# Optimization experiments

Measured on AMD Instinct MI355X. Metric: run time of the kernel, lower is better.

## Reference

```python
import jax, jax.numpy as jnp
import numpy as np

B, N, E, V, D, H = 16, 4096, 524288, 4, 64, 128
MLP_IN = H + 3 + 2  # node feats + conditioning coords + two temperature scalars
SRC_T, TGT_T = 300.0, 600.0
SCALE_RANGE = 0.5


def _w(k, shape):
    return (jax.random.normal(k, shape, jnp.float32) / np.sqrt(shape[0])).astype(jnp.float32)


def setup_inputs() -> dict:
    key = jax.random.key(0)
    ks = jax.random.split(key, 32)
    inp = {
        "coordinates": jax.random.normal(ks[0], (B, N, 3), jnp.float32),
        "atom_types": jax.random.randint(ks[1], (B, N), 0, V, jnp.int32),
        "adj_list": jax.random.randint(ks[2], (E, 2), 0, N, jnp.int32),
        "edge_batch_idx": jax.random.randint(ks[3], (E,), 0, B, jnp.int32),
        "masked_elements": jnp.zeros((B, N), bool),
        # message-passing GNN params
        "embed": jax.random.normal(ks[4], (V, D), jnp.float32),
        "W_in": _w(ks[5], (D + 3, H)), "b_in": jnp.zeros(H, jnp.float32),
        "W_msg0": _w(ks[6], (2 * H, H)), "b_msg0": jnp.zeros(H, jnp.float32),
        "W_upd0": _w(ks[7], (2 * H, H)), "b_upd0": jnp.zeros(H, jnp.float32),
        "W_msg1": _w(ks[8], (2 * H, H)), "b_msg1": jnp.zeros(H, jnp.float32),
        "W_upd1": _w(ks[9], (2 * H, H)), "b_upd1": jnp.zeros(H, jnp.float32),
        "W_out": _w(ks[10], (H, H)), "b_out": jnp.zeros(H, jnp.float32),
        # scale MLP (random small weights instead of zero init so output is non-trivial)
        "Ws0": _w(ks[11], (MLP_IN, H)), "bs0": jnp.zeros(H, jnp.float32),
        "Ws1": _w(ks[12], (H, H)), "bs1": jnp.zeros(H, jnp.float32),
        "Ws2": _w(ks[13], (H, H // 2)), "bs2": jnp.zeros(H // 2, jnp.float32),
        "Ws3": _w(ks[14], (H // 2, 3)) * 0.1, "bs3": jnp.zeros(3, jnp.float32),
        # shift MLP
        "Wt0": _w(ks[15], (MLP_IN, H)), "bt0": jnp.zeros(H, jnp.float32),
        "Wt1": _w(ks[16], (H, H)), "bt1": jnp.zeros(H, jnp.float32),
        "Wt2": _w(ks[17], (H, H // 2)), "bt2": jnp.zeros(H // 2, jnp.float32),
        "Wt3": _w(ks[18], (H // 2, 3)) * 0.1, "bt3": jnp.zeros(3, jnp.float32),
    }
    return inp


def _mlp(x, layers):
    for Wl, bl in layers[:-1]:
        x = jax.nn.relu(x @ Wl + bl)
    Wl, bl = layers[-1]
    return x @ Wl + bl


def reference(coordinates, atom_types, adj_list, edge_batch_idx, masked_elements,
              embed, W_in, b_in, W_msg0, b_msg0, W_upd0, b_upd0,
              W_msg1, b_msg1, W_upd1, b_upd1, W_out, b_out,
              Ws0, bs0, Ws1, bs1, Ws2, bs2, Ws3, bs3,
              Wt0, bt0, Wt1, bt1, Wt2, bt2, Wt3, bt3):
    Bn, Nn, _ = coordinates.shape
    valid = ~masked_elements                              # [B,N]
    vf = valid[..., None].astype(coordinates.dtype)
    # ---- message passing GNN ----
    h = jnp.concatenate([embed[atom_types], coordinates], -1)  # [B,N,D+3]
    h = jax.nn.relu(h @ W_in + b_in) * vf
    hf = h.reshape(Bn * Nn, -1)
    src = edge_batch_idx * Nn + adj_list[:, 0]
    dst = edge_batch_idx * Nn + adj_list[:, 1]
    for Wm, bm, Wu, bu in ((W_msg0, b_msg0, W_upd0, b_upd0),
                           (W_msg1, b_msg1, W_upd1, b_upd1)):
        m = jax.nn.relu(jnp.concatenate([hf[src], hf[dst]], -1) @ Wm + bm)  # [E,H]
        agg = jax.ops.segment_sum(m, dst, num_segments=Bn * Nn)             # [B*N,H]
        hf = jax.nn.relu(jnp.concatenate([hf, agg], -1) @ Wu + bu)
    node_feats = (hf @ W_out + b_out).reshape(Bn, Nn, -1) * vf              # [B,N,H]
    # ---- coupling transform (phase=0: atoms with type>0 are transformed) ----
    coupling = (atom_types > 0) & valid                  # [B,N]
    cond = coordinates * (~coupling)[..., None].astype(coordinates.dtype)
    temps = jnp.broadcast_to(jnp.asarray([SRC_T, TGT_T], coordinates.dtype), (Bn, Nn, 2))
    x = jnp.concatenate([node_feats, cond, temps], -1)   # [B,N,H+5]
    raw_scales = _mlp(x, [(Ws0, bs0), (Ws1, bs1), (Ws2, bs2), (Ws3, bs3)])
    shifts = _mlp(x, [(Wt0, bt0), (Wt1, bt1), (Wt2, bt2), (Wt3, bt3)])
    m3 = coupling[..., None].astype(coordinates.dtype)   # [B,N,1]
    log_scales = jnp.tanh(raw_scales) * SCALE_RANGE * m3 * vf
    shifts = shifts * m3
    log_det = log_scales.sum((1, 2))                     # [B]
    out = jnp.exp(log_scales) * coordinates + shifts
    out = jnp.where(coupling[..., None], out, coordinates)
    return out, log_det
```

## Files before the change

### kernel.cpp

```cpp
#include <hip/hip_runtime.h>

#define NB    16
#define NN    4096
#define NNODE (NB*NN)
#define NE    524288

typedef __attribute__((ext_vector_type(8))) short bf16x8_t;
typedef __attribute__((ext_vector_type(4))) float f32x4_t;

__device__ __forceinline__ unsigned short f2bf(float f) {
    union { float f; unsigned u; } v; v.f = f;
    return (unsigned short)((v.u + 0x7FFFu + ((v.u >> 16) & 1u)) >> 16);
}
__device__ __forceinline__ float bf2f(unsigned short h) {
    union { unsigned u; float f; } v; v.u = ((unsigned)h) << 16;
    return v.f;
}

__global__ void deg_k(const int* __restrict__ adj, const int* __restrict__ ebi, int* __restrict__ deg)
{
    int e = blockIdx.x * 256 + threadIdx.x;
    atomicAdd(&deg[ebi[e] * NN + adj[2 * e + 1]], 1);
}

// ... 65 lines not shown
        int n = idx >> 7, k = idx & 127;
        WoutP[n * 128 + k] = f2bf(Wout[k * 128 + n]);
    } else if (bid < 768) {
        int idx = (bid - 576) * 256 + tx;
        int n = idx / 192, kk = idx % 192;
        const float* W = n < 128 ? Ws0 : Wt0;
        int nn = n & 127;
        Bt0cat[n * 192 + kk] = f2bf(kk < 133 ? W[kk * 128 + nn] : 0.f);
    } else if (bid < 896) {
        int idx = (bid - 768) * 256 + tx;
        int n = idx >> 7, k = idx & 127;
        const float* W = n < 128 ? Ws1 : Wt1;
        Bt1cat[n * 128 + k] = f2bf(W[k * 128 + (n & 127)]);
    } else if (bid < 1024) {
        int idx = (bid - 896) * 256 + tx;
        int n = idx >> 7, k = idx & 127;
        const float* W = n < 128 ? Ws2 : Wt2;
        int nn = n & 127;
        Bt2cat[n * 128 + k] = f2bf(nn < 64 ? W[k * 64 + nn] : 0.f);
    } else if (bid == 1024) {
        b0cat[tx] = (tx < 128) ? bs0[tx] : bt0[tx - 128];
    } else if (bid == 1025) {
        b1cat[tx] = (tx < 128) ? bs1[tx] : bt1[tx - 128];
    } else if (bid == 1026) {
        int nn = tx & 127;
        b2cat[tx] = (nn < 64) ? ((tx < 128) ? bs2[nn] : bt2[nn]) : 0.f;
    } else if (bid == 1027) {
        bm0cat[tx] = (tx < 128) ? 0.f : bm0[tx - 128];
    } else {
        bm1cat[tx] = (tx < 128) ? 0.f : bm1[tx - 128];
    }
}

__device__ __forceinline__ void msg_phase(const char* act, char* Bs,
    const unsigned short* __restrict__ Bt, const float* __restrict__ bias,
    unsigned short* __restrict__ P12, size_t row0, int tx)
{
    const int wid = tx >> 6, l = tx & 63;
    const int wr = wid >> 1, wc = wid & 1;
    const int rsel = l & 15, kq = l >> 4;
    const int rg = l >> 4, cc = l & 15;
#pragma unroll
    for (int nh = 0; nh < 2; ++nh) {
        f32x4_t acc[2][4];
#pragma unroll
        for (int i = 0; i < 2; ++i)
#pragma unroll
            for (int j = 0; j < 4; ++j) { f32x4_t z = {0.f,0.f,0.f,0.f}; acc[i][j] = z; }
#pragma unroll
        for (int kc = 0; kc < 128; kc += 64) {
            __syncthreads();
#pragma unroll
            for (int p = 0; p < 4; ++p) {
                int idx = tx + p * 256;
                int n = idx >> 3, kg = idx & 7;
                uint4 v = *(const uint4*)(Bt + (size_t)(nh * 128 + n) * 128 + kc + kg * 8);
                *(uint4*)(Bs + n * 128 + ((kg * 16) ^ ((n & 7) << 4))) = v;
            }
            __syncthreads();
#pragma unroll
            for (int ks = 0; ks < 2; ++ks) {
                bf16x8_t af[2], bv[4];
#pragma unroll
                for (int fm = 0; fm < 2; ++fm) {
                    int r = wr * 32 + fm * 16 + rsel;
                    af[fm] = *(const bf16x8_t*)(act + r * 256 + kc * 2 + ((ks * 64 + kq * 16) ^ ((r & 7) << 4)));
                }
#pragma unroll
                for (int fn = 0; fn < 4; ++fn) {
                    int n = wc * 64 + fn * 16 + rsel;
                    bv[fn] = *(const bf16x8_t*)(Bs + n * 128 + ((ks * 64 + kq * 16) ^ ((n & 7) << 4)));
                }
#pragma unroll
                for (int fm = 0; fm < 2; ++fm)
#pragma unroll
                    for (int fn = 0; fn < 4; ++fn)
                        acc[fm][fn] = __builtin_amdgcn_mfma_f32_16x16x32_bf16(af[fm], bv[fn], acc[fm][fn], 0, 0, 0);
            }
        }
        __syncthreads();
#pragma unroll
        for (int fm = 0; fm < 2; ++fm)
#pragma unroll
            for (int rr = 0; rr < 4; ++rr) {
                int row = wr * 32 + fm * 16 + rg * 4 + rr;
#pragma unroll
                for (int fn = 0; fn < 4; ++fn) {
                    int col = wc * 64 + fn * 16 + cc;
                    float v = acc[fm][fn][rr] + bias[nh * 128 + col];
                    int cb = col * 2;
                    *(unsigned short*)(Bs + row * 256 + (cb & ~127) + ((cb & 127) ^ ((row & 7) << 4))) = f2bf(v);
                }
            }
        __syncthreads();
#pragma unroll
        for (int p = 0; p < 4; ++p) {
            int idx = tx + p * 256;
            int row = idx >> 4, g = idx & 15;
            int pb = g * 16;
            uint4 v = *(const uint4*)(Bs + row * 256 + (pb & ~127) + ((pb & 127) ^ ((row & 7) << 4)));
            *(uint4*)(P12 + (row0 + row) * 256 + nh * 128 + g * 8) = v;
        }
    }
}

__launch_bounds__(256, 4)
__global__ void fused_im_k(const int* __restrict__ types, const float* __restrict__ coords,
                           const unsigned char* __restrict__ maskb,
                           const float* __restrict__ embed, const float* __restrict__ W_in,
                           const float* __restrict__ b_in,
                           const unsigned short* __restrict__ Btm, const float* __restrict__ bmcat,
                           unsigned short* __restrict__ hf, unsigned short* __restrict__ P12)
{
    __shared__ __align__(16) char act[16384];
    __shared__ __align__(16) char Bs[16384];
    const int tx = threadIdx.x;
    const size_t row0 = (size_t)blockIdx.x * 64;

    float* wf = (float*)Bs;
    float* xs = (float*)(Bs + 4096);
#pragma unroll
    for (int p = 0; p < 4; ++p) {
        int idx = tx + p * 256;
        int k = idx >> 7, c = idx & 127;
        wf[idx] = (k < 7) ? W_in[k * 128 + c] : b_in[c];
    }
    if (tx < 64) {
        size_t node = row0 + tx;
        int tp = types[node];
#pragma unroll
        for (int j = 0; j < 4; ++j) xs[tx * 8 + j] = embed[(size_t)tp * 4 + j];
#pragma unroll
        for (int j = 0; j < 3; ++j) xs[tx * 8 + 4 + j] = coords[node * 3 + j];
    }
    __syncthreads();
    {
        int row = tx >> 2, c0 = (tx & 3) * 32;
        float x0 = xs[row*8+0], x1 = xs[row*8+1], x2 = xs[row*8+2], x3 = xs[row*8+3];
        float x4 = xs[row*8+4], x5 = xs[row*8+5], x6 = xs[row*8+6];
        bool msk = maskb[row0 + row];
        int swz = (row & 7) << 4;
#pragma unroll
        for (int c = 0; c < 32; ++c) {
            int col = c0 + c;
            float a = wf[7*128+col] + x0*wf[col] + x1*wf[128+col] + x2*wf[256+col]
                    + x3*wf[384+col] + x4*wf[512+col] + x5*wf[640+col] + x6*wf[768+col];
            a = msk ? 0.f : fmaxf(a, 0.f);
            int cb = col * 2;
            *(unsigned short*)(act + row * 256 + (cb & ~127) + ((cb & 127) ^ swz)) = f2bf(a);
        }
    }
    __syncthreads();
#pragma unroll
    for (int p = 0; p < 4; ++p) {
        int idx = tx + p * 256;
        int row = idx >> 4, g = idx & 15;
        int pb = g * 16;
        uint4 v = *(const uint4*)(act + row * 256 + (pb & ~127) + ((pb & 127) ^ ((row & 7) << 4)));
        *(uint4*)(hf + (row0 + row) * 128 + g * 8) = v;
    }
    msg_phase(act, Bs, Btm, bmcat, P12, row0, tx);
}

__launch_bounds__(256, 4)
__global__ void fused_um_k(const unsigned short* __restrict__ hfin,
                           const unsigned short* __restrict__ aggp,
                           const unsigned short* __restrict__ Btu, const float* __restrict__ bu,
                           const unsigned short* __restrict__ Btm, const float* __restrict__ bmcat,
                           unsigned short* __restrict__ hfout, unsigned short* __restrict__ P12)
{
    __shared__ __align__(16) char act[16384];
    __shared__ __align__(16) char Bs[16384];
    const int tx = threadIdx.x;
    const int wid = tx >> 6, l = tx & 63;
    const int wr = wid >> 1, wc = wid & 1;
    const int rsel = l & 15, kq = l >> 4, rg = l >> 4, cc = l & 15;
    const size_t row0 = (size_t)blockIdx.x * 64;

    f32x4_t acc[2][4];
#pragma unroll
    for (int i = 0; i < 2; ++i)
#pragma unroll
        for (int j = 0; j < 4; ++j) { f32x4_t z = {0.f,0.f,0.f,0.f}; acc[i][j] = z; }
#pragma unroll
    for (int kc = 0; kc < 256; kc += 64) {
        const unsigned short* Ap = (kc < 128) ? hfin : aggp;
        int kloc = (kc < 128) ? kc : kc - 128;
        __syncthreads();
#pragma unroll
        for (int p = 0; p < 4; ++p) {
            int idx = tx + p * 256;
            int n = idx >> 3, kg = idx & 7;
            uint4 v = *(const uint4*)(Btu + (size_t)n * 256 + kc + kg * 8);
            *(uint4*)(Bs + n * 128 + ((kg * 16) ^ ((n & 7) << 4))) = v;
        }
        __syncthreads();
#pragma unroll
        for (int ks = 0; ks < 2; ++ks) {
            bf16x8_t af[2], bv[4];
#pragma unroll
            for (int fm = 0; fm < 2; ++fm) {
                size_t r = row0 + wr * 32 + fm * 16 + rsel;
                af[fm] = *(const bf16x8_t*)(Ap + r * 128 + kloc + ks * 32 + kq * 8);
            }
#pragma unroll
            for (int fn = 0; fn < 4; ++fn) {
                int n = wc * 64 + fn * 16 + rsel;
                bv[fn] = *(const bf16x8_t*)(Bs + n * 128 + ((ks * 64 + kq * 16) ^ ((n & 7) << 4)));
            }
#pragma unroll
            for (int fm = 0; fm < 2; ++fm)
#pragma unroll
                for (int fn = 0; fn < 4; ++fn)
                    acc[fm][fn] = __builtin_amdgcn_mfma_f32_16x16x32_bf16(af[fm], bv[fn], acc[fm][fn], 0, 0, 0);
        }
    }
#pragma unroll
    for (int fm = 0; fm < 2; ++fm)
#pragma unroll
        for (int rr = 0; rr < 4; ++rr) {
            int row = wr * 32 + fm * 16 + rg * 4 + rr;
#pragma unroll
            for (int fn = 0; fn < 4; ++fn) {
                int col = wc * 64 + fn * 16 + cc;
                float v = fmaxf(acc[fm][fn][rr] + bu[col], 0.f);
                int cb = col * 2;
                *(unsigned short*)(act + row * 256 + (cb & ~127) + ((cb & 127) ^ ((row & 7) << 4))) = f2bf(v);
            }
        }
    __syncthreads();
#pragma unroll
    for (int p = 0; p < 4; ++p) {
        int idx = tx + p * 256;
        int row = idx >> 4, g = idx & 15;
        int pb = g * 16;
        uint4 v = *(const uint4*)(act + row * 256 + (pb & ~127) + ((pb & 127) ^ ((row & 7) << 4)));
        *(uint4*)(hfout + (row0 + row) * 128 + g * 8) = v;
    }
    msg_phase(act, Bs, Btm, bmcat, P12, row0, tx);
}

__global__ void agg_k(const unsigned short* __restrict__ P12,
                      const int* __restrict__ offs, const int* __restrict__ esrc,
                      unsigned short* __restrict__ agg)
{
    int bid = blockIdx.x;
    int chunk = gridDim.x >> 3;
    int swz = (bid & 7) * chunk + (bid >> 3);
    int node = swz * 4 + (threadIdx.x >> 6);
    int l = threadIdx.x & 63;
    int beg = offs[node], end = offs[node + 1];
    unsigned p2w = *(const unsigned*)(P12 + (size_t)node * 256 + 128 + 2 * l);
    float p2a = bf2f((unsigned short)(p2w & 0xFFFF));
    float p2b = bf2f((unsigned short)(p2w >> 16));
    float aa = 0.f, ab = 0.f;
    int i = beg;
    for (; i + 3 < end; i += 4) {
        int s0 = esrc[i], s1 = esrc[i+1], s2 = esrc[i+2], s3 = esrc[i+3];
        unsigned v0 = *(const unsigned*)(P12 + (size_t)s0 * 256 + 2 * l);
        unsigned v1 = *(const unsigned*)(P12 + (size_t)s1 * 256 + 2 * l);
        unsigned v2 = *(const unsigned*)(P12 + (size_t)s2 * 256 + 2 * l);
        unsigned v3 = *(const unsigned*)(P12 + (size_t)s3 * 256 + 2 * l);
        aa += fmaxf(bf2f((unsigned short)(v0 & 0xFFFF)) + p2a, 0.f);
        ab += fmaxf(bf2f((unsigned short)(v0 >> 16))    + p2b, 0.f);
        aa += fmaxf(bf2f((unsigned short)(v1 & 0xFFFF)) + p2a, 0.f);
        ab += fmaxf(bf2f((unsigned short)(v1 >> 16))    + p2b, 0.f);
        aa += fmaxf(bf2f((unsigned short)(v2 & 0xFFFF)) + p2a, 0.f);
        ab += fmaxf(bf2f((unsigned short)(v2 >> 16))    + p2b, 0.f);
        aa += fmaxf(bf2f((unsigned short)(v3 & 0xFFFF)) + p2a, 0.f);
        ab += fmaxf(bf2f((unsigned short)(v3 >> 16))    + p2b, 0.f);
    }
    for (; i < end; ++i) {
        int s0 = esrc[i];
        unsigned v0 = *(const unsigned*)(P12 + (size_t)s0 * 256 + 2 * l);
        aa += fmaxf(bf2f((unsigned short)(v0 & 0xFFFF)) + p2a, 0.f);
        ab += fmaxf(bf2f((unsigned short)(v0 >> 16))    + p2b, 0.f);
    }
    unsigned o = (unsigned)f2bf(aa) | ((unsigned)f2bf(ab) << 16);
    *(unsigned*)(agg + (size_t)node * 128 + 2 * l) = o;
}

__launch_bounds__(256, 2)
__global__ void fused_ut_k(const unsigned short* __restrict__ hfin,
                           const unsigned short* __restrict__ aggp,
                           const unsigned short* __restrict__ Btu, const float* __restrict__ bu,
                           const unsigned short* __restrict__ WoutP, const float* __restrict__ bOut,
                           const unsigned short* __restrict__ Bt0, const float* __restrict__ b0,
                           const unsigned short* __restrict__ Bt1, const float* __restrict__ b1,
                           const unsigned short* __restrict__ Bt2, const float* __restrict__ b2,
                           const float* __restrict__ Ws3, const float* __restrict__ bs3,
                           const float* __restrict__ Wt3, const float* __restrict__ bt3,
                           const float* __restrict__ coords, const int* __restrict__ types,
                           const unsigned char* __restrict__ maskb,
                           float* __restrict__ outc, float* __restrict__ partial)
{
    __shared__ __align__(16) char act[32768];
    __shared__ __align__(16) char hfn[16384];
    __shared__ __align__(16) char Bs[32768];
    const int tx = threadIdx.x;
    const int wid = tx >> 6, l = tx & 63;
    const int rsel = l & 15, kq = l >> 4, rg = l >> 4, cc = l & 15;
    const size_t row0 = (size_t)blockIdx.x * 64;

    {
        const int wr = wid >> 1, wc = wid & 1;
        f32x4_t acc[2][4];
#pragma unroll
        for (int i = 0; i < 2; ++i)
#pragma unroll
            for (int j = 0; j < 4; ++j) { f32x4_t z = {0.f,0.f,0.f,0.f}; acc[i][j] = z; }
#pragma unroll
        for (int kc = 0; kc < 256; kc += 64) {
            const unsigned short* Ap = (kc < 128) ? hfin : aggp;
            int kloc = (kc < 128) ? kc : kc - 128;
            __syncthreads();
#pragma unroll
            for (int p = 0; p < 4; ++p) {
                int idx = tx + p * 256;
                int n = idx >> 3, kg = idx & 7;
                uint4 v = *(const uint4*)(Btu + (size_t)n * 256 + kc + kg * 8);
                *(uint4*)(Bs + n * 128 + ((kg * 16) ^ ((n & 7) << 4))) = v;
            }
            __syncthreads();
#pragma unroll
            for (int ks = 0; ks < 2; ++ks) {
                bf16x8_t af[2], bv[4];
#pragma unroll
                for (int fm = 0; fm < 2; ++fm) {
                    size_t r = row0 + wr * 32 + fm * 16 + rsel;
                    af[fm] = *(const bf16x8_t*)(Ap + r * 128 + kloc + ks * 32 + kq * 8);
                }
#pragma unroll
                for (int fn = 0; fn < 4; ++fn) {
                    int n = wc * 64 + fn * 16 + rsel;
                    bv[fn] = *(const bf16x8_t*)(Bs + n * 128 + ((ks * 64 + kq * 16) ^ ((n & 7) << 4)));
                }
#pragma unroll
                for (int fm = 0; fm < 2; ++fm)
#pragma unroll
                    for (int fn = 0; fn < 4; ++fn)
                        acc[fm][fn] = __builtin_amdgcn_mfma_f32_16x16x32_bf16(af[fm], bv[fn], acc[fm][fn], 0, 0, 0);
            }
        }
#pragma unroll
        for (int fm = 0; fm < 2; ++fm)
#pragma unroll
            for (int rr = 0; rr < 4; ++rr) {
                int row = wr * 32 + fm * 16 + rg * 4 + rr;
#pragma unroll
                for (int fn = 0; fn < 4; ++fn) {
                    int col = wc * 64 + fn * 16 + cc;
                    float v = fmaxf(acc[fm][fn][rr] + bu[col], 0.f);
                    int cb = col * 2;
                    *(unsigned short*)(hfn + row * 256 + (cb & ~127) + ((cb & 127) ^ ((row & 7) << 4))) = f2bf(v);
                }
            }
    }
    __syncthreads();

    {
        const int wr = wid >> 1, wc = wid & 1;
        f32x4_t acc[2][4];
#pragma unroll
        for (int i = 0; i < 2; ++i)
#pragma unroll
            for (int j = 0; j < 4; ++j) { f32x4_t z = {0.f,0.f,0.f,0.f}; acc[i][j] = z; }
#pragma unroll
        for (int kc = 0; kc < 128; kc += 64) {
            __syncthreads();
#pragma unroll
            for (int p = 0; p < 4; ++p) {
                int idx = tx + p * 256;
                int n = idx >> 3, kg = idx & 7;
                uint4 v = *(const uint4*)(WoutP + (size_t)n * 128 + kc + kg * 8);
                *(uint4*)(Bs + n * 128 + ((kg * 16) ^ ((n & 7) << 4))) = v;
            }
            __syncthreads();
#pragma unroll
            for (int ks = 0; ks < 2; ++ks) {
                bf16x8_t af[2], bv[4];
#pragma unroll
                for (int fm = 0; fm < 2; ++fm) {
                    int r = wr * 32 + fm * 16 + rsel;
                    af[fm] = *(const bf16x8_t*)(hfn + r * 256 + kc * 2 + ((ks * 64 + kq * 16) ^ ((r & 7) << 4)));
                }
#pragma unroll
                for (int fn = 0; fn < 4; ++fn) {
                    int n = wc * 64 + fn * 16 + rsel;
                    bv[fn] = *(const bf16x8_t*)(Bs + n * 128 + ((ks * 64 + kq * 16) ^ ((n & 7) << 4)));
                }
#pragma unroll
                for (int fm = 0; fm < 2; ++fm)
#pragma unroll
                    for (int fn = 0; fn < 4; ++fn)
                        acc[fm][fn] = __builtin_amdgcn_mfma_f32_16x16x32_bf16(af[fm], bv[fn], acc[fm][fn], 0, 0, 0);
            }
        }
#pragma unroll
        for (int fm = 0; fm < 2; ++fm)
#pragma unroll
            for (int rr = 0; rr < 4; ++rr) {
                int row = wr * 32 + fm * 16 + rg * 4 + rr;
                bool zero = maskb[row0 + row];
#pragma unroll
                for (int fn = 0; fn < 4; ++fn) {
                    int col = wc * 64 + fn * 16 + cc;
                    float v = acc[fm][fn][rr] + bOut[col];
                    if (zero) v = 0.f;
                    int cb = col * 2;
                    *(unsigned short*)(act + row * 512 + (cb & ~127) + ((cb & 127) ^ ((row & 7) << 4))) = f2bf(v);
                }
            }
    }
#pragma unroll
    for (int p = 0; p < 16; ++p) {
        int idx = tx + p * 256;
        int row = idx >> 6, ci = idx & 63;
        int col = 128 + ci;
        size_t node = row0 + row;
        bool coup = (types[node] > 0) && !maskb[node];
        float v;
        if (ci < 3)       v = coup ? 0.f : coords[node * 3 + ci];
        else if (ci == 3) v = 300.f;
        else if (ci == 4) v = 600.f;
        else              v = 0.f;
        int cb = col * 2;
        *(unsigned short*)(act + row * 512 + (cb & ~127) + ((cb & 127) ^ ((row & 7) << 4))) = f2bf(v);
    }
    __syncthreads();

    const int wr = wid >> 1, wc = wid & 1;
#pragma unroll
    for (int layer = 0; layer < 3; ++layer) {
        const unsigned short* Bt = layer == 0 ? Bt0 : (layer == 1 ? Bt1 : Bt2);
        const float* bb = layer == 0 ? b0 : (layer == 1 ? b1 : b2);
        const int ldbt = layer == 0 ? 192 : 128;
        const int Ktot = layer == 0 ? 192 : 128;
        const int kbase = (layer == 0) ? 0 : (wc ? 256 : 0);
        f32x4_t acc[2][8];
#pragma unroll
        for (int i = 0; i < 2; ++i)
#pragma unroll
            for (int j = 0; j < 8; ++j) { f32x4_t z = {0.f,0.f,0.f,0.f}; acc[i][j] = z; }
        for (int kc = 0; kc < Ktot; kc += 64) {
            __syncthreads();
#pragma unroll
            for (int p = 0; p < 8; ++p) {
                int idx = tx + p * 256;
                int n = idx >> 3, kg = idx & 7;
                uint4 v = *(const uint4*)(Bt + (size_t)n * ldbt + kc + kg * 8);
                *(uint4*)(Bs + n * 128 + ((kg * 16) ^ ((n & 7) << 4))) = v;
            }
            __syncthreads();
#pragma unroll
            for (int ks = 0; ks < 2; ++ks) {
                bf16x8_t af[2], bv[8];
#pragma unroll
                for (int fm = 0; fm < 2; ++fm) {
                    int r = wr * 32 + fm * 16 + rsel;
                    af[fm] = *(const bf16x8_t*)(act + r * 512 + kbase + kc * 2 + ((ks * 64 + kq * 16) ^ ((r & 7) << 4)));
                }
#pragma unroll
                for (int fn = 0; fn < 8; ++fn) {
                    int n = wc * 128 + fn * 16 + rsel;
                    bv[fn] = *(const bf16x8_t*)(Bs + n * 128 + ((ks * 64 + kq * 16) ^ ((n & 7) << 4)));
                }
#pragma unroll
                for (int fm = 0; fm < 2; ++fm)
#pragma unroll
                    for (int fn = 0; fn < 8; ++fn)
                        acc[fm][fn] = __builtin_amdgcn_mfma_f32_16x16x32_bf16(af[fm], bv[fn], acc[fm][fn], 0, 0, 0);
            }
        }
        __syncthreads();
#pragma unroll
        for (int fm = 0; fm < 2; ++fm)
#pragma unroll
            for (int rr = 0; rr < 4; ++rr) {
                int row = wr * 32 + fm * 16 + rg * 4 + rr;
#pragma unroll
                for (int fn = 0; fn < 8; ++fn) {
                    int col = wc * 128 + fn * 16 + cc;
                    float v = fmaxf(acc[fm][fn][rr] + bb[col], 0.f);
                    int cb = col * 2;
                    *(unsigned short*)(act + row * 512 + (cb & ~127) + ((cb & 127) ^ ((row & 7) << 4))) = f2bf(v);
                }
            }
        __syncthreads();
    }

    float* W3f = (float*)hfn;
    float* red = (float*)(hfn + 2048);
    for (int i = tx; i < 384; i += 256)
        W3f[i] = (i < 192) ? Ws3[i] : Wt3[i - 192];
    __syncthreads();
    {
        int row = tx >> 2, sub = tx & 3;
        int swz = (row & 7) << 4;
        float rs0 = 0.f, rs1 = 0.f, rs2 = 0.f, sh0 = 0.f, sh1 = 0.f, sh2 = 0.f;
#pragma unroll
        for (int kk = 0; kk < 16; ++kk) {
            int k = sub * 16 + kk;
            float av = bf2f(*(const unsigned short*)(act + row * 512 + ((k * 2) ^ swz)));
            float bv = bf2f(*(const unsigned short*)(act + row * 512 + 256 + ((k * 2) ^ swz)));
            rs0 += av * W3f[k * 3 + 0]; rs1 += av * W3f[k * 3 + 1]; rs2 += av * W3f[k * 3 + 2];
            sh0 += bv * W3f[192 + k * 3 + 0]; sh1 += bv * W3f[192 + k * 3 + 1]; sh2 += bv * W3f[192 + k * 3 + 2];
        }
        rs0 += __shfl_xor(rs0, 1); rs0 += __shfl_xor(rs0, 2);
        rs1 += __shfl_xor(rs1, 1); rs1 += __shfl_xor(rs1, 2);
        rs2 += __shfl_xor(rs2, 1); rs2 += __shfl_xor(rs2, 2);
        sh0 += __shfl_xor(sh0, 1); sh0 += __shfl_xor(sh0, 2);
        sh1 += __shfl_xor(sh1, 1); sh1 += __shfl_xor(sh1, 2);
        sh2 += __shfl_xor(sh2, 1); sh2 += __shfl_xor(sh2, 2);
        if (sub == 0) {
            size_t node = row0 + row;
            bool coup = (types[node] > 0) && !maskb[node];
            float c0 = coords[node * 3 + 0], c1 = coords[node * 3 + 1], c2 = coords[node * 3 + 2];
            float ls0 = 0.f, ls1 = 0.f, ls2 = 0.f, o0 = c0, o1 = c1, o2 = c2;
            if (coup) {
                ls0 = tanhf(rs0 + bs3[0]) * 0.5f;
// ... 68 lines not shown
    int*   offs = (int*)alloc((size_t)(NNODE + 1) * 4);
    int*   cur  = (int*)alloc((size_t)NNODE * 4);
    int*   esrc = (int*)alloc((size_t)NE * 4);
    unsigned short* Btm0 = (unsigned short*)alloc(256 * 128 * 2);
    unsigned short* Btm1 = (unsigned short*)alloc(256 * 128 * 2);
    unsigned short* Btu0 = (unsigned short*)alloc(128 * 256 * 2);
    unsigned short* Btu1 = (unsigned short*)alloc(128 * 256 * 2);
    unsigned short* WoutP  = (unsigned short*)alloc(128 * 128 * 2);
    unsigned short* Bt0cat = (unsigned short*)alloc(256 * 192 * 2);
    unsigned short* Bt1cat = (unsigned short*)alloc(256 * 128 * 2);
    unsigned short* Bt2cat = (unsigned short*)alloc(256 * 128 * 2);
    float* b0cat  = (float*)alloc(256 * 4);
    float* b1cat  = (float*)alloc(256 * 4);
    float* b2cat  = (float*)alloc(256 * 4);
    float* bm0cat = (float*)alloc(256 * 4);
    float* bm1cat = (float*)alloc(256 * 4);
    float* partial = (float*)alloc(1024 * 4);

    hipMemsetAsync(deg, 0, (size_t)NNODE * 4, stream);
    hipMemsetAsync(cur, 0, (size_t)NNODE * 4, stream);

    deg_k<<<NE / 256, 256, 0, stream>>>(adj, ebi, deg);
    scan_k<<<1, 1024, 0, stream>>>(deg, offs);
    scat_k<<<NE / 256, 256, 0, stream>>>(adj, ebi, offs, cur, esrc);
    prep_k<<<1029, 256, 0, stream>>>(W_msg[0], W_msg[1], W_upd[0], W_upd[1], W_out,
                                     Ws0, Wt0, Ws1, Wt1, Ws2, Wt2,
                                     bs0, bt0, bs1, bt1, bs2, bt2, b_msg[0], b_msg[1],
                                     Btm0, Btm1, Btu0, Btu1, WoutP,
                                     Bt0cat, Bt1cat, Bt2cat,
                                     b0cat, b1cat, b2cat, bm0cat, bm1cat);

    fused_im_k<<<1024, 256, 0, stream>>>(types, coords, maskb, embed, W_in, b_in,
                                         Btm0, bm0cat, hf, P12);
    agg_k<<<NNODE / 4, 256, 0, stream>>>(P12, offs, esrc, agg);
    fused_um_k<<<1024, 256, 0, stream>>>(hf, agg, Btu0, b_upd[0], Btm1, bm1cat, hf, P12);
    agg_k<<<NNODE / 4, 256, 0, stream>>>(P12, offs, esrc, agg);

    float* outc = (float*)d_out;
    fused_ut_k<<<1024, 256, 0, stream>>>(hf, agg, Btu1, b_upd[1], WoutP, b_out,
                                         Bt0cat, b0cat, Bt1cat, b1cat, Bt2cat, b2cat,
                                         Ws3, bs3, Wt3, bt3,
                                         coords, types, maskb, outc, partial);
    red_k<<<1, 256, 0, stream>>>(partial, outc + (size_t)NNODE * 3);
}
```

Baseline: 260.1 us.

## Load GEMM weight fragments directly from global memory instead of staging through LDS

Every MFMA GEMM loop in the message, update and tail kernels now reads its B-operand fragments straight from global memory (served by L1/L2 for the small, shared weight matrices) instead of copying weight tiles into a shared Bs buffer with two barriers per K-chunk. This removes the per-chunk LDS staging stores and __syncthreads, and drops the 32 KB Bs buffer from the tail kernel. The tail kernel's launch bound is raised from 2 to 3 blocks per CU to use the freed LDS. The cost is more global/cache load traffic per wave, with longer load latency sitting directly in front of the MFMAs and no software prefetch to hide it.

```diff
diff --git a/kernel.cpp b/kernel.cpp
--- a/kernel.cpp
+++ b/kernel.cpp
@@ -121,7 +121,7 @@
     }
 }
 
-__device__ __forceinline__ void msg_phase(const char* act, char* Bs,
+__device__ __forceinline__ void msg_phase(const char* act, char* buf,
     const unsigned short* __restrict__ Bt, const float* __restrict__ bias,
     unsigned short* __restrict__ P12, size_t row0, int tx)
 {
@@ -137,35 +137,24 @@
 #pragma unroll
             for (int j = 0; j < 4; ++j) { f32x4_t z = {0.f,0.f,0.f,0.f}; acc[i][j] = z; }
 #pragma unroll
-        for (int kc = 0; kc < 128; kc += 64) {
-            __syncthreads();
-#pragma unroll
-            for (int p = 0; p < 4; ++p) {
-                int idx = tx + p * 256;
-                int n = idx >> 3, kg = idx & 7;
-                uint4 v = *(const uint4*)(Bt + (size_t)(nh * 128 + n) * 128 + kc + kg * 8);
-                *(uint4*)(Bs + n * 128 + ((kg * 16) ^ ((n & 7) << 4))) = v;
-            }
-            __syncthreads();
-#pragma unroll
-            for (int ks = 0; ks < 2; ++ks) {
-                bf16x8_t af[2], bv[4];
-#pragma unroll
-                for (int fm = 0; fm < 2; ++fm) {
-                    int r = wr * 32 + fm * 16 + rsel;
-                    af[fm] = *(const bf16x8_t*)(act + r * 256 + kc * 2 + ((ks * 64 + kq * 16) ^ ((r & 7) << 4)));
-                }
-#pragma unroll
-                for (int fn = 0; fn < 4; ++fn) {
-                    int n = wc * 64 + fn * 16 + rsel;
-                    bv[fn] = *(const bf16x8_t*)(Bs + n * 128 + ((ks * 64 + kq * 16) ^ ((n & 7) << 4)));
-                }
-#pragma unroll
-                for (int fm = 0; fm < 2; ++fm)
-#pragma unroll
-                    for (int fn = 0; fn < 4; ++fn)
-                        acc[fm][fn] = __builtin_amdgcn_mfma_f32_16x16x32_bf16(af[fm], bv[fn], acc[fm][fn], 0, 0, 0);
-            }
+        for (int kk = 0; kk < 128; kk += 32) {
+            bf16x8_t af[2], bv[4];
+#pragma unroll
+            for (int fm = 0; fm < 2; ++fm) {
+                int r = wr * 32 + fm * 16 + rsel;
+                int ab = (kk + kq * 8) * 2;
+                af[fm] = *(const bf16x8_t*)(act + r * 256 + (ab & ~127) + ((ab & 127) ^ ((r & 7) << 4)));
+            }
+#pragma unroll
+            for (int fn = 0; fn < 4; ++fn) {
+                int n = nh * 128 + wc * 64 + fn * 16 + rsel;
+                bv[fn] = *(const bf16x8_t*)(Bt + (size_t)n * 128 + kk + kq * 8);
+            }
+#pragma unroll
+            for (int fm = 0; fm < 2; ++fm)
+#pragma unroll
+                for (int fn = 0; fn < 4; ++fn)
+                    acc[fm][fn] = __builtin_amdgcn_mfma_f32_16x16x32_bf16(af[fm], bv[fn], acc[fm][fn], 0, 0, 0);
         }
         __syncthreads();
 #pragma unroll
@@ -178,7 +167,7 @@
                     int col = wc * 64 + fn * 16 + cc;
                     float v = acc[fm][fn][rr] + bias[nh * 128 + col];
                     int cb = col * 2;
-                    *(unsigned short*)(Bs + row * 256 + (cb & ~127) + ((cb & 127) ^ ((row & 7) << 4))) = f2bf(v);
+                    *(unsigned short*)(buf + row * 256 + (cb & ~127) + ((cb & 127) ^ ((row & 7) << 4))) = f2bf(v);
                 }
             }
         __syncthreads();
@@ -187,7 +176,7 @@
             int idx = tx + p * 256;
             int row = idx >> 4, g = idx & 15;
             int pb = g * 16;
-            uint4 v = *(const uint4*)(Bs + row * 256 + (pb & ~127) + ((pb & 127) ^ ((row & 7) << 4)));
+            uint4 v = *(const uint4*)(buf + row * 256 + (pb & ~127) + ((pb & 127) ^ ((row & 7) << 4)));
             *(uint4*)(P12 + (row0 + row) * 256 + nh * 128 + g * 8) = v;
         }
     }
@@ -202,12 +191,12 @@
                            unsigned short* __restrict__ hf, unsigned short* __restrict__ P12)
 {
     __shared__ __align__(16) char act[16384];
-    __shared__ __align__(16) char Bs[16384];
+    __shared__ __align__(16) char buf[16384];
     const int tx = threadIdx.x;
     const size_t row0 = (size_t)blockIdx.x * 64;
 
-    float* wf = (float*)Bs;
-    float* xs = (float*)(Bs + 4096);
+    float* wf = (float*)buf;
+    float* xs = (float*)(buf + 4096);
 #pragma unroll
     for (int p = 0; p < 4; ++p) {
         int idx = tx + p * 256;
@@ -248,7 +237,7 @@
         uint4 v = *(const uint4*)(act + row * 256 + (pb & ~127) + ((pb & 127) ^ ((row & 7) << 4)));
         *(uint4*)(hf + (row0 + row) * 128 + g * 8) = v;
     }
-    msg_phase(act, Bs, Btm, bmcat, P12, row0, tx);
+    msg_phase(act, buf, Btm, bmcat, P12, row0, tx);
 }
 
 __launch_bounds__(256, 4)
@@ -259,7 +248,7 @@
                            unsigned short* __restrict__ hfout, unsigned short* __restrict__ P12)
 {
     __shared__ __align__(16) char act[16384];
-    __shared__ __align__(16) char Bs[16384];
+    __shared__ __align__(16) char buf[16384];
     const int tx = threadIdx.x;
     const int wid = tx >> 6, l = tx & 63;
     const int wr = wid >> 1, wc = wid & 1;
@@ -272,37 +261,25 @@
 #pragma unroll
         for (int j = 0; j < 4; ++j) { f32x4_t z = {0.f,0.f,0.f,0.f}; acc[i][j] = z; }
 #pragma unroll
-    for (int kc = 0; kc < 256; kc += 64) {
-        const unsigned short* Ap = (kc < 128) ? hfin : aggp;
-        int kloc = (kc < 128) ? kc : kc - 128;
-        __syncthreads();
-#pragma unroll
-        for (int p = 0; p < 4; ++p) {
-            int idx = tx + p * 256;
-            int n = idx >> 3, kg = idx & 7;
-            uint4 v = *(const uint4*)(Btu + (size_t)n * 256 + kc + kg * 8);
-            *(uint4*)(Bs + n * 128 + ((kg * 16) ^ ((n & 7) << 4))) = v;
-        }
-        __syncthreads();
-#pragma unroll
-        for (int ks = 0; ks < 2; ++ks) {
-            bf16x8_t af[2], bv[4];
-#pragma unroll
-            for (int fm = 0; fm < 2; ++fm) {
-                size_t r = row0 + wr * 32 + fm * 16 + rsel;
-                af[fm] = *(const bf16x8_t*)(Ap + r * 128 + kloc + ks * 32 + kq * 8);
-            }
-#pragma unroll
-            for (int fn = 0; fn < 4; ++fn) {
-                int n = wc * 64 + fn * 16 + rsel;
-                bv[fn] = *(const bf16x8_t*)(Bs + n * 128 + ((ks * 64 + kq * 16) ^ ((n & 7) << 4)));
-            }
-#pragma unroll
-            for (int fm = 0; fm < 2; ++fm)
-#pragma unroll
-                for (int fn = 0; fn < 4; ++fn)
-                    acc[fm][fn] = __builtin_amdgcn_mfma_f32_16x16x32_bf16(af[fm], bv[fn], acc[fm][fn], 0, 0, 0);
-        }
+    for (int kk = 0; kk < 256; kk += 32) {
+        const unsigned short* Ap = (kk < 128) ? hfin : aggp;
+        int kloc = kk & 127;
+        bf16x8_t af[2], bv[4];
+#pragma unroll
+        for (int fm = 0; fm < 2; ++fm) {
+            size_t r = row0 + wr * 32 + fm * 16 + rsel;
+            af[fm] = *(const bf16x8_t*)(Ap + r * 128 + kloc + kq * 8);
+        }
+#pragma unroll
+        for (int fn = 0; fn < 4; ++fn) {
+            int n = wc * 64 + fn * 16 + rsel;
+            bv[fn] = *(const bf16x8_t*)(Btu + (size_t)n * 256 + kk + kq * 8);
+        }
+#pragma unroll
+        for (int fm = 0; fm < 2; ++fm)
+#pragma unroll
+            for (int fn = 0; fn < 4; ++fn)
+                acc[fm][fn] = __builtin_amdgcn_mfma_f32_16x16x32_bf16(af[fm], bv[fn], acc[fm][fn], 0, 0, 0);
     }
 #pragma unroll
     for (int fm = 0; fm < 2; ++fm)
@@ -326,7 +303,7 @@
         uint4 v = *(const uint4*)(act + row * 256 + (pb & ~127) + ((pb & 127) ^ ((row & 7) << 4)));
         *(uint4*)(hfout + (row0 + row) * 128 + g * 8) = v;
     }
-    msg_phase(act, Bs, Btm, bmcat, P12, row0, tx);
+    msg_phase(act, buf, Btm, bmcat, P12, row0, tx);
 }
 
 __global__ void agg_k(const unsigned short* __restrict__ P12,
@@ -369,7 +346,7 @@
     *(unsigned*)(agg + (size_t)node * 128 + 2 * l) = o;
 }
 
-__launch_bounds__(256, 2)
+__launch_bounds__(256, 3)
 __global__ void fused_ut_k(const unsigned short* __restrict__ hfin,
                            const unsigned short* __restrict__ aggp,
                            const unsigned short* __restrict__ Btu, const float* __restrict__ bu,
@@ -385,51 +362,38 @@
 {
     __shared__ __align__(16) char act[32768];
     __shared__ __align__(16) char hfn[16384];
-    __shared__ __align__(16) char Bs[32768];
     const int tx = threadIdx.x;
     const int wid = tx >> 6, l = tx & 63;
     const int rsel = l & 15, kq = l >> 4, rg = l >> 4, cc = l & 15;
     const size_t row0 = (size_t)blockIdx.x * 64;
+    const int wr = wid >> 1, wc = wid & 1;
 
     {
-        const int wr = wid >> 1, wc = wid & 1;
         f32x4_t acc[2][4];
 #pragma unroll
         for (int i = 0; i < 2; ++i)
 #pragma unroll
             for (int j = 0; j < 4; ++j) { f32x4_t z = {0.f,0.f,0.f,0.f}; acc[i][j] = z; }
 #pragma unroll
-        for (int kc = 0; kc < 256; kc += 64) {
-            const unsigned short* Ap = (kc < 128) ? hfin : aggp;
-            int kloc = (kc < 128) ? kc : kc - 128;
-            __syncthreads();
-#pragma unroll
-            for (int p = 0; p < 4; ++p) {
-                int idx = tx + p * 256;
-                int n = idx >> 3, kg = idx & 7;
-                uint4 v = *(const uint4*)(Btu + (size_t)n * 256 + kc + kg * 8);
-                *(uint4*)(Bs + n * 128 + ((kg * 16) ^ ((n & 7) << 4))) = v;
-            }
-            __syncthreads();
-#pragma unroll
-            for (int ks = 0; ks < 2; ++ks) {
-                bf16x8_t af[2], bv[4];
-#pragma unroll
-                for (int fm = 0; fm < 2; ++fm) {
-                    size_t r = row0 + wr * 32 + fm * 16 + rsel;
-                    af[fm] = *(const bf16x8_t*)(Ap + r * 128 + kloc + ks * 32 + kq * 8);
-                }
-#pragma unroll
-                for (int fn = 0; fn < 4; ++fn) {
-                    int n = wc * 64 + fn * 16 + rsel;
-                    bv[fn] = *(const bf16x8_t*)(Bs + n * 128 + ((ks * 64 + kq * 16) ^ ((n & 7) << 4)));
-                }
-#pragma unroll
-                for (int fm = 0; fm < 2; ++fm)
-#pragma unroll
-                    for (int fn = 0; fn < 4; ++fn)
-                        acc[fm][fn] = __builtin_amdgcn_mfma_f32_16x16x32_bf16(af[fm], bv[fn], acc[fm][fn], 0, 0, 0);
-            }
+        for (int kk = 0; kk < 256; kk += 32) {
+            const unsigned short* Ap = (kk < 128) ? hfin : aggp;
+            int kloc = kk & 127;
+            bf16x8_t af[2], bv[4];
+#pragma unroll
+            for (int fm = 0; fm < 2; ++fm) {
+                size_t r = row0 + wr * 32 + fm * 16 + rsel;
+                af[fm] = *(const bf16x8_t*)(Ap + r * 128 + kloc + kq * 8);
+            }
+#pragma unroll
+            for (int fn = 0; fn < 4; ++fn) {
+                int n = wc * 64 + fn * 16 + rsel;
+                bv[fn] = *(const bf16x8_t*)(Btu + (size_t)n * 256 + kk + kq * 8);
+            }
+#pragma unroll
+            for (int fm = 0; fm < 2; ++fm)
+#pragma unroll
+                for (int fn = 0; fn < 4; ++fn)
+                    acc[fm][fn] = __builtin_amdgcn_mfma_f32_16x16x32_bf16(af[fm], bv[fn], acc[fm][fn], 0, 0, 0);
         }
 #pragma unroll
         for (int fm = 0; fm < 2; ++fm)
@@ -448,42 +412,30 @@
     __syncthreads();
 
     {
-        const int wr = wid >> 1, wc = wid & 1;
         f32x4_t acc[2][4];
 #pragma unroll
         for (int i = 0; i < 2; ++i)
 #pragma unroll
             for (int j = 0; j < 4; ++j) { f32x4_t z = {0.f,0.f,0.f,0.f}; acc[i][j] = z; }
 #pragma unroll
-        for (int kc = 0; kc < 128; kc += 64) {
-            __syncthreads();
-#pragma unroll
-            for (int p = 0; p < 4; ++p) {
-                int idx = tx + p * 256;
-                int n = idx >> 3, kg = idx & 7;
-                uint4 v = *(const uint4*)(WoutP + (size_t)n * 128 + kc + kg * 8);
-                *(uint4*)(Bs + n * 128 + ((kg * 16) ^ ((n & 7) << 4))) = v;
-            }
-            __syncthreads();
-#pragma unroll
-            for (int ks = 0; ks < 2; ++ks) {
-                bf16x8_t af[2], bv[4];
-#pragma unroll
-                for (int fm = 0; fm < 2; ++fm) {
-                    int r = wr * 32 + fm * 16 + rsel;
-                    af[fm] = *(const bf16x8_t*)(hfn + r * 256 + kc * 2 + ((ks * 64 + kq * 16) ^ ((r & 7) << 4)));
-                }
-#pragma unroll
-                for (int fn = 0; fn < 4; ++fn) {
-                    int n = wc * 64 + fn * 16 + rsel;
-                    bv[fn] = *(const bf16x8_t*)(Bs + n * 128 + ((ks * 64 + kq * 16) ^ ((n & 7) << 4)));
-                }
-#pragma unroll
-                for (int fm = 0; fm < 2; ++fm)
-#pragma unroll
-                    for (int fn = 0; fn < 4; ++fn)
-                        acc[fm][fn] = __builtin_amdgcn_mfma_f32_16x16x32_bf16(af[fm], bv[fn], acc[fm][fn], 0, 0, 0);
-            }
+        for (int kk = 0; kk < 128; kk += 32) {
+            bf16x8_t af[2], bv[4];
+#pragma unroll
+            for (int fm = 0; fm < 2; ++fm) {
+                int r = wr * 32 + fm * 16 + rsel;
+                int ab = (kk + kq * 8) * 2;
+                af[fm] = *(const bf16x8_t*)(hfn + r * 256 + (ab & ~127) + ((ab & 127) ^ ((r & 7) << 4)));
+            }
+#pragma unroll
+            for (int fn = 0; fn < 4; ++fn) {
+                int n = wc * 64 + fn * 16 + rsel;
+                bv[fn] = *(const bf16x8_t*)(WoutP + (size_t)n * 128 + kk + kq * 8);
+            }
+#pragma unroll
+            for (int fm = 0; fm < 2; ++fm)
+#pragma unroll
+                for (int fn = 0; fn < 4; ++fn)
+                    acc[fm][fn] = __builtin_amdgcn_mfma_f32_16x16x32_bf16(af[fm], bv[fn], acc[fm][fn], 0, 0, 0);
         }
 #pragma unroll
         for (int fm = 0; fm < 2; ++fm)
@@ -518,7 +470,6 @@
     }
     __syncthreads();
 
-    const int wr = wid >> 1, wc = wid & 1;
 #pragma unroll
     for (int layer = 0; layer < 3; ++layer) {
         const unsigned short* Bt = layer == 0 ? Bt0 : (layer == 1 ? Bt1 : Bt2);
@@ -531,35 +482,24 @@
         for (int i = 0; i < 2; ++i)
 #pragma unroll
             for (int j = 0; j < 8; ++j) { f32x4_t z = {0.f,0.f,0.f,0.f}; acc[i][j] = z; }
-        for (int kc = 0; kc < Ktot; kc += 64) {
-            __syncthreads();
-#pragma unroll
-            for (int p = 0; p < 8; ++p) {
-                int idx = tx + p * 256;
-                int n = idx >> 3, kg = idx & 7;
-                uint4 v = *(const uint4*)(Bt + (size_t)n * ldbt + kc + kg * 8);
-                *(uint4*)(Bs + n * 128 + ((kg * 16) ^ ((n & 7) << 4))) = v;
-            }
-            __syncthreads();
-#pragma unroll
-            for (int ks = 0; ks < 2; ++ks) {
-                bf16x8_t af[2], bv[8];
-#pragma unroll
-                for (int fm = 0; fm < 2; ++fm) {
-                    int r = wr * 32 + fm * 16 + rsel;
-                    af[fm] = *(const bf16x8_t*)(act + r * 512 + kbase + kc * 2 + ((ks * 64 + kq * 16) ^ ((r & 7) << 4)));
-                }
-#pragma unroll
-                for (int fn = 0; fn < 8; ++fn) {
-                    int n = wc * 128 + fn * 16 + rsel;
-                    bv[fn] = *(const bf16x8_t*)(Bs + n * 128 + ((ks * 64 + kq * 16) ^ ((n & 7) << 4)));
-                }
-#pragma unroll
-                for (int fm = 0; fm < 2; ++fm)
-#pragma unroll
-                    for (int fn = 0; fn < 8; ++fn)
-                        acc[fm][fn] = __builtin_amdgcn_mfma_f32_16x16x32_bf16(af[fm], bv[fn], acc[fm][fn], 0, 0, 0);
-            }
+        for (int kk = 0; kk < Ktot; kk += 32) {
+            bf16x8_t af[2], bv[8];
+#pragma unroll
+            for (int fm = 0; fm < 2; ++fm) {
+                int r = wr * 32 + fm * 16 + rsel;
+                int ab = (kk + kq * 8) * 2;
+                af[fm] = *(const bf16x8_t*)(act + r * 512 + kbase + (ab & ~127) + ((ab & 127) ^ ((r & 7) << 4)));
+            }
+#pragma unroll
+            for (int fn = 0; fn < 8; ++fn) {
+                int n = wc * 128 + fn * 16 + rsel;
+                bv[fn] = *(const bf16x8_t*)(Bt + (size_t)n * ldbt + kk + kq * 8);
+            }
+#pragma unroll
+            for (int fm = 0; fm < 2; ++fm)
+#pragma unroll
+                for (int fn = 0; fn < 8; ++fn)
+                    acc[fm][fn] = __builtin_amdgcn_mfma_f32_16x16x32_bf16(af[fm], bv[fn], acc[fm][fn], 0, 0, 0);
         }
         __syncthreads();
 #pragma unroll
```

Result: slower. 367.8 us (+41.4%).

## Halve agg threads per node with wider loads; cut fused_ut LDS for occupancy

Applied to the files above, without the earlier changes.

The aggregation kernel now gives each node 32 lanes that each load 8 bytes (four bf16 features) per neighbour, so one block covers 8 nodes and launches half as many blocks. The final fused update/MLP kernel drops its separate 32 KB B-tile buffer: it reuses the activation buffer for the first GEMMs and splits the MLP layer GEMMs into two 128-column halves staged through the 16 KB hfn buffer. Launch bounds are raised to 3 blocks per SM to raise occupancy. This adds extra barriers and half-width tile reloads, and staging B into act before act holds the activations depends on the exact order of barriers.

```diff
diff --git a/kernel.cpp b/kernel.cpp
--- a/kernel.cpp
+++ b/kernel.cpp
@@ -274,7 +274,7 @@
 #pragma unroll
     for (int kc = 0; kc < 256; kc += 64) {
         const unsigned short* Ap = (kc < 128) ? hfin : aggp;
-        int kloc = (kc < 128) ? kc : kc - 128;
+        int kloc = kc & 127;
         __syncthreads();
 #pragma unroll
         for (int p = 0; p < 4; ++p) {
@@ -336,40 +336,54 @@
     int bid = blockIdx.x;
     int chunk = gridDim.x >> 3;
     int swz = (bid & 7) * chunk + (bid >> 3);
-    int node = swz * 4 + (threadIdx.x >> 6);
-    int l = threadIdx.x & 63;
+    int node = swz * 8 + (threadIdx.x >> 5);
+    int l = threadIdx.x & 31;
     int beg = offs[node], end = offs[node + 1];
-    unsigned p2w = *(const unsigned*)(P12 + (size_t)node * 256 + 128 + 2 * l);
-    float p2a = bf2f((unsigned short)(p2w & 0xFFFF));
-    float p2b = bf2f((unsigned short)(p2w >> 16));
-    float aa = 0.f, ab = 0.f;
+    uint2 p2w = *(const uint2*)(P12 + (size_t)node * 256 + 128 + 4 * l);
+    float p2a = bf2f((unsigned short)(p2w.x & 0xFFFF));
+    float p2b = bf2f((unsigned short)(p2w.x >> 16));
+    float p2c = bf2f((unsigned short)(p2w.y & 0xFFFF));
+    float p2d = bf2f((unsigned short)(p2w.y >> 16));
+    float aa = 0.f, ab = 0.f, ac = 0.f, ad = 0.f;
     int i = beg;
     for (; i + 3 < end; i += 4) {
         int s0 = esrc[i], s1 = esrc[i+1], s2 = esrc[i+2], s3 = esrc[i+3];
-        unsigned v0 = *(const unsigned*)(P12 + (size_t)s0 * 256 + 2 * l);
-        unsigned v1 = *(const unsigned*)(P12 + (size_t)s1 * 256 + 2 * l);
-        unsigned v2 = *(const unsigned*)(P12 + (size_t)s2 * 256 + 2 * l);
-        unsigned v3 = *(const unsigned*)(P12 + (size_t)s3 * 256 + 2 * l);
-        aa += fmaxf(bf2f((unsigned short)(v0 & 0xFFFF)) + p2a, 0.f);
-        ab += fmaxf(bf2f((unsigned short)(v0 >> 16))    + p2b, 0.f);
-        aa += fmaxf(bf2f((unsigned short)(v1 & 0xFFFF)) + p2a, 0.f);
-        ab += fmaxf(bf2f((unsigned short)(v1 >> 16))    + p2b, 0.f);
-        aa += fmaxf(bf2f((unsigned short)(v2 & 0xFFFF)) + p2a, 0.f);
-        ab += fmaxf(bf2f((unsigned short)(v2 >> 16))    + p2b, 0.f);
-        aa += fmaxf(bf2f((unsigned short)(v3 & 0xFFFF)) + p2a, 0.f);
-        ab += fmaxf(bf2f((unsigned short)(v3 >> 16))    + p2b, 0.f);
+        uint2 v0 = *(const uint2*)(P12 + (size_t)s0 * 256 + 4 * l);
+        uint2 v1 = *(const uint2*)(P12 + (size_t)s1 * 256 + 4 * l);
+        uint2 v2 = *(const uint2*)(P12 + (size_t)s2 * 256 + 4 * l);
+        uint2 v3 = *(const uint2*)(P12 + (size_t)s3 * 256 + 4 * l);
+        aa += fmaxf(bf2f((unsigned short)(v0.x & 0xFFFF)) + p2a, 0.f);
+        ab += fmaxf(bf2f((unsigned short)(v0.x >> 16))    + p2b, 0.f);
+        ac += fmaxf(bf2f((unsigned short)(v0.y & 0xFFFF)) + p2c, 0.f);
+        ad += fmaxf(bf2f((unsigned short)(v0.y >> 16))    + p2d, 0.f);
+        aa += fmaxf(bf2f((unsigned short)(v1.x & 0xFFFF)) + p2a, 0.f);
+        ab += fmaxf(bf2f((unsigned short)(v1.x >> 16))    + p2b, 0.f);
+        ac += fmaxf(bf2f((unsigned short)(v1.y & 0xFFFF)) + p2c, 0.f);
+        ad += fmaxf(bf2f((unsigned short)(v1.y >> 16))    + p2d, 0.f);
+        aa += fmaxf(bf2f((unsigned short)(v2.x & 0xFFFF)) + p2a, 0.f);
+        ab += fmaxf(bf2f((unsigned short)(v2.x >> 16))    + p2b, 0.f);
+        ac += fmaxf(bf2f((unsigned short)(v2.y & 0xFFFF)) + p2c, 0.f);
+        ad += fmaxf(bf2f((unsigned short)(v2.y >> 16))    + p2d, 0.f);
+        aa += fmaxf(bf2f((unsigned short)(v3.x & 0xFFFF)) + p2a, 0.f);
+        ab += fmaxf(bf2f((unsigned short)(v3.x >> 16))    + p2b, 0.f);
+        ac += fmaxf(bf2f((unsigned short)(v3.y & 0xFFFF)) + p2c, 0.f);
+        ad += fmaxf(bf2f((unsigned short)(v3.y >> 16))    + p2d, 0.f);
     }
     for (; i < end; ++i) {
         int s0 = esrc[i];
-        unsigned v0 = *(const unsigned*)(P12 + (size_t)s0 * 256 + 2 * l);
-        aa += fmaxf(bf2f((unsigned short)(v0 & 0xFFFF)) + p2a, 0.f);
-        ab += fmaxf(bf2f((unsigned short)(v0 >> 16))    + p2b, 0.f);
-    }
-    unsigned o = (unsigned)f2bf(aa) | ((unsigned)f2bf(ab) << 16);
-    *(unsigned*)(agg + (size_t)node * 128 + 2 * l) = o;
-}
-
-__launch_bounds__(256, 2)
+        uint2 v0 = *(const uint2*)(P12 + (size_t)s0 * 256 + 4 * l);
+        aa += fmaxf(bf2f((unsigned short)(v0.x & 0xFFFF)) + p2a, 0.f);
+        ab += fmaxf(bf2f((unsigned short)(v0.x >> 16))    + p2b, 0.f);
+        ac += fmaxf(bf2f((unsigned short)(v0.y & 0xFFFF)) + p2c, 0.f);
+        ad += fmaxf(bf2f((unsigned short)(v0.y >> 16))    + p2d, 0.f);
+    }
+    uint2 o;
+    o.x = (unsigned)f2bf(aa) | ((unsigned)f2bf(ab) << 16);
+    o.y = (unsigned)f2bf(ac) | ((unsigned)f2bf(ad) << 16);
+    *(uint2*)(agg + (size_t)node * 128 + 4 * l) = o;
+}
+
+__launch_bounds__(256, 3)
 __global__ void fused_ut_k(const unsigned short* __restrict__ hfin,
                            const unsigned short* __restrict__ aggp,
                            const unsigned short* __restrict__ Btu, const float* __restrict__ bu,
@@ -385,14 +399,13 @@
 {
     __shared__ __align__(16) char act[32768];
     __shared__ __align__(16) char hfn[16384];
-    __shared__ __align__(16) char Bs[32768];
     const int tx = threadIdx.x;
     const int wid = tx >> 6, l = tx & 63;
     const int rsel = l & 15, kq = l >> 4, rg = l >> 4, cc = l & 15;
     const size_t row0 = (size_t)blockIdx.x * 64;
+    const int wr = wid >> 1, wc = wid & 1;
 
     {
-        const int wr = wid >> 1, wc = wid & 1;
         f32x4_t acc[2][4];
 #pragma unroll
         for (int i = 0; i < 2; ++i)
@@ -401,14 +414,14 @@
 #pragma unroll
         for (int kc = 0; kc < 256; kc += 64) {
             const unsigned short* Ap = (kc < 128) ? hfin : aggp;
-            int kloc = (kc < 128) ? kc : kc - 128;
+            int kloc = kc & 127;
             __syncthreads();
 #pragma unroll
             for (int p = 0; p < 4; ++p) {
                 int idx = tx + p * 256;
                 int n = idx >> 3, kg = idx & 7;
                 uint4 v = *(const uint4*)(Btu + (size_t)n * 256 + kc + kg * 8);
-                *(uint4*)(Bs + n * 128 + ((kg * 16) ^ ((n & 7) << 4))) = v;
+                *(uint4*)(act + n * 128 + ((kg * 16) ^ ((n & 7) << 4))) = v;
             }
             __syncthreads();
 #pragma unroll
@@ -422,7 +435,7 @@
 #pragma unroll
                 for (int fn = 0; fn < 4; ++fn) {
                     int n = wc * 64 + fn * 16 + rsel;
-                    bv[fn] = *(const bf16x8_t*)(Bs + n * 128 + ((ks * 64 + kq * 16) ^ ((n & 7) << 4)));
+                    bv[fn] = *(const bf16x8_t*)(act + n * 128 + ((ks * 64 + kq * 16) ^ ((n & 7) << 4)));
                 }
 #pragma unroll
                 for (int fm = 0; fm < 2; ++fm)
@@ -445,10 +458,8 @@
                 }
             }
     }
-    __syncthreads();
 
     {
-        const int wr = wid >> 1, wc = wid & 1;
         f32x4_t acc[2][4];
 #pragma unroll
         for (int i = 0; i < 2; ++i)
@@ -462,7 +473,7 @@
                 int idx = tx + p * 256;
                 int n = idx >> 3, kg = idx & 7;
                 uint4 v = *(const uint4*)(WoutP + (size_t)n * 128 + kc + kg * 8);
-                *(uint4*)(Bs + n * 128 + ((kg * 16) ^ ((n & 7) << 4))) = v;
+                *(uint4*)(act + n * 128 + ((kg * 16) ^ ((n & 7) << 4))) = v;
             }
             __syncthreads();
 #pragma unroll
@@ -476,7 +487,7 @@
 #pragma unroll
                 for (int fn = 0; fn < 4; ++fn) {
                     int n = wc * 64 + fn * 16 + rsel;
-                    bv[fn] = *(const bf16x8_t*)(Bs + n * 128 + ((ks * 64 + kq * 16) ^ ((n & 7) << 4)));
+                    bv[fn] = *(const bf16x8_t*)(act + n * 128 + ((ks * 64 + kq * 16) ^ ((n & 7) << 4)));
                 }
 #pragma unroll
                 for (int fm = 0; fm < 2; ++fm)
@@ -485,6 +496,7 @@
                         acc[fm][fn] = __builtin_amdgcn_mfma_f32_16x16x32_bf16(af[fm], bv[fn], acc[fm][fn], 0, 0, 0);
             }
         }
+        __syncthreads();
 #pragma unroll
         for (int fm = 0; fm < 2; ++fm)
 #pragma unroll
@@ -518,63 +530,69 @@
     }
     __syncthreads();
 
-    const int wr = wid >> 1, wc = wid & 1;
 #pragma unroll
     for (int layer = 0; layer < 3; ++layer) {
         const unsigned short* Bt = layer == 0 ? Bt0 : (layer == 1 ? Bt1 : Bt2);
         const float* bb = layer == 0 ? b0 : (layer == 1 ? b1 : b2);
         const int ldbt = layer == 0 ? 192 : 128;
         const int Ktot = layer == 0 ? 192 : 128;
-        const int kbase = (layer == 0) ? 0 : (wc ? 256 : 0);
-        f32x4_t acc[2][8];
-#pragma unroll
-        for (int i = 0; i < 2; ++i)
-#pragma unroll
-            for (int j = 0; j < 8; ++j) { f32x4_t z = {0.f,0.f,0.f,0.f}; acc[i][j] = z; }
+        f32x4_t acc[2][2][4];
+#pragma unroll
+        for (int h = 0; h < 2; ++h)
+#pragma unroll
+            for (int i = 0; i < 2; ++i)
+#pragma unroll
+                for (int j = 0; j < 4; ++j) { f32x4_t z = {0.f,0.f,0.f,0.f}; acc[h][i][j] = z; }
         for (int kc = 0; kc < Ktot; kc += 64) {
-            __syncthreads();
-#pragma unroll
-            for (int p = 0; p < 8; ++p) {
-                int idx = tx + p * 256;
-                int n = idx >> 3, kg = idx & 7;
-                uint4 v = *(const uint4*)(Bt + (size_t)n * ldbt + kc + kg * 8);
-                *(uint4*)(Bs + n * 128 + ((kg * 16) ^ ((n & 7) << 4))) = v;
-            }
-            __syncthreads();
-#pragma unroll
-            for (int ks = 0; ks < 2; ++ks) {
-                bf16x8_t af[2], bv[8];
-#pragma unroll
-                for (int fm = 0; fm < 2; ++fm) {
-                    int r = wr * 32 + fm * 16 + rsel;
-                    af[fm] = *(const bf16x8_t*)(act + r * 512 + kbase + kc * 2 + ((ks * 64 + kq * 16) ^ ((r & 7) << 4)));
-                }
-#pragma unroll
-                for (int fn = 0; fn < 8; ++fn) {
-                    int n = wc * 128 + fn * 16 + rsel;
-                    bv[fn] = *(const bf16x8_t*)(Bs + n * 128 + ((ks * 64 + kq * 16) ^ ((n & 7) << 4)));
-                }
-#pragma unroll
-                for (int fm = 0; fm < 2; ++fm)
-#pragma unroll
-                    for (int fn = 0; fn < 8; ++fn)
-                        acc[fm][fn] = __builtin_amdgcn_mfma_f32_16x16x32_bf16(af[fm], bv[fn], acc[fm][fn], 0, 0, 0);
-            }
-        }
-        __syncthreads();
-#pragma unroll
-        for (int fm = 0; fm < 2; ++fm)
-#pragma unroll
-            for (int rr = 0; rr < 4; ++rr) {
-                int row = wr * 32 + fm * 16 + rg * 4 + rr;
-#pragma unroll
-                for (int fn = 0; fn < 8; ++fn) {
-                    int col = wc * 128 + fn * 16 + cc;
-                    float v = fmaxf(acc[fm][fn][rr] + bb[col], 0.f);
-                    int cb = col * 2;
-                    *(unsigned short*)(act + row * 512 + (cb & ~127) + ((cb & 127) ^ ((row & 7) << 4))) = f2bf(v);
-                }
-            }
+#pragma unroll
+            for (int h = 0; h < 2; ++h) {
+                __syncthreads();
+#pragma unroll
+                for (int p = 0; p < 4; ++p) {
+                    int idx = tx + p * 256;
+                    int n = idx >> 3, kg = idx & 7;
+                    uint4 v = *(const uint4*)(Bt + (size_t)(h * 128 + n) * ldbt + kc + kg * 8);
+                    *(uint4*)(hfn + n * 128 + ((kg * 16) ^ ((n & 7) << 4))) = v;
+                }
+                __syncthreads();
+                const int kbase = (layer == 0) ? 0 : (h ? 256 : 0);
+#pragma unroll
+                for (int ks = 0; ks < 2; ++ks) {
+                    bf16x8_t af[2], bv[4];
+#pragma unroll
+                    for (int fm = 0; fm < 2; ++fm) {
+                        int r = wr * 32 + fm * 16 + rsel;
+                        af[fm] = *(const bf16x8_t*)(act + r * 512 + kbase + kc * 2 + ((ks * 64 + kq * 16) ^ ((r & 7) << 4)));
+                    }
+#pragma unroll
+                    for (int fn = 0; fn < 4; ++fn) {
+                        int n = wc * 64 + fn * 16 + rsel;
+                        bv[fn] = *(const bf16x8_t*)(hfn + n * 128 + ((ks * 64 + kq * 16) ^ ((n & 7) << 4)));
+                    }
+#pragma unroll
+                    for (int fm = 0; fm < 2; ++fm)
+#pragma unroll
+                        for (int fn = 0; fn < 4; ++fn)
+                            acc[h][fm][fn] = __builtin_amdgcn_mfma_f32_16x16x32_bf16(af[fm], bv[fn], acc[h][fm][fn], 0, 0, 0);
+                }
+            }
+        }
+        __syncthreads();
+#pragma unroll
+        for (int h = 0; h < 2; ++h)
+#pragma unroll
+            for (int fm = 0; fm < 2; ++fm)
+#pragma unroll
+                for (int rr = 0; rr < 4; ++rr) {
+                    int row = wr * 32 + fm * 16 + rg * 4 + rr;
+#pragma unroll
+                    for (int fn = 0; fn < 4; ++fn) {
+                        int col = h * 128 + wc * 64 + fn * 16 + cc;
+                        float v = fmaxf(acc[h][fm][fn][rr] + bb[col], 0.f);
+                        int cb = col * 2;
+                        *(unsigned short*)(act + row * 512 + (cb & ~127) + ((cb & 127) ^ ((row & 7) << 4))) = f2bf(v);
+                    }
+                }
         __syncthreads();
     }
 
@@ -709,9 +727,9 @@
 
     fused_im_k<<<1024, 256, 0, stream>>>(types, coords, maskb, embed, W_in, b_in,
                                          Btm0, bm0cat, hf, P12);
-    agg_k<<<NNODE / 4, 256, 0, stream>>>(P12, offs, esrc, agg);
+    agg_k<<<NNODE / 8, 256, 0, stream>>>(P12, offs, esrc, agg);
     fused_um_k<<<1024, 256, 0, stream>>>(hf, agg, Btu0, b_upd[0], Btm1, bm1cat, hf, P12);
-    agg_k<<<NNODE / 4, 256, 0, stream>>>(P12, offs, esrc, agg);
+    agg_k<<<NNODE / 8, 256, 0, stream>>>(P12, offs, esrc, agg);
 
     float* outc = (float*)d_out;
     fused_ut_k<<<1024, 256, 0, stream>>>(hf, agg, Btu1, b_upd[1], WoutP, b_out,
```

Result: slower. 291.4 us (+12.0%).
